# Performance work log

Measured on AMD Instinct MI355X. Metric: run time of the kernel, lower is better.

Reference implementation:

```python
import jax, jax.numpy as jnp
import numpy as np

B, S, H = 32, 512, 768
NHEAD, DH = 8, 96          # 8 heads * 96 = 768
E = 4096                   # edges per sample
NC = 2
NEG = -1e9
EPS = 1e-5


def _p(k, shape, scale=0.02):
    return scale * jax.random.normal(k, shape, dtype=jnp.float32)


def setup_inputs() -> dict:
    key = jax.random.key(0)
    ks = jax.random.split(key, 24)
    z = lambda *s: jnp.zeros(s, jnp.float32)
    return {
        "diff_encoded": jax.random.normal(ks[0], (B, S, H), jnp.float32),
        "msg_encoded": jax.random.normal(ks[1], (B, S, H), jnp.float32),
        "msg_mask": jnp.ones((B, S), jnp.int32),
        "edge_index_diff": jax.random.randint(ks[2], (B, 2, E), 0, S),
        "edge_index_msg": jax.random.randint(ks[3], (B, 2, E), 0, S),
        # GATv2Conv(heads=1): lin_l (source/message), lin_r (target), att vector, output bias
        "gat_wl": _p(ks[4], (H, H)), "gat_bl": z(H),
        "gat_wr": _p(ks[5], (H, H)), "gat_br": z(H),
        "gat_att": _p(ks[6], (H,)), "gat_bias": z(H),
        # cross MultiheadAttention
        "wq": _p(ks[7], (H, H)), "bq": z(H),
        "wk": _p(ks[8], (H, H)), "bk": z(H),
        "wv": _p(ks[9], (H, H)), "bv": z(H),
        "wo": _p(ks[10], (H, H)), "bo": z(H),
        # LayerNorm + MLP head
        "ln_g": jnp.ones((H,), jnp.float32), "ln_b": z(H),
        "fc0_w": _p(ks[11], (H, 512)), "fc0_b": z(512),
        "fc1_w": _p(ks[12], (512, 128)), "fc1_b": z(128),
        "fc2_w": _p(ks[13], (128, NC)), "fc2_b": z(NC),
    }


def _gat_single(x, edges, wl, bl, wr, br, att, bias):
    # GATv2Conv, heads=1, add_self_loops=True. x: [N,H], edges: [2,E] (src, dst).
    N = x.shape[0]
    src, dst = edges[0], edges[1]
    valid = (src < N) & (dst < N)            # clip_edge_index, as a mask
    src = jnp.where(valid, src, 0)
    dst = jnp.where(valid, dst, 0)
    loop = jnp.arange(N, dtype=src.dtype)    # PyG adds self loops
    src_a = jnp.concatenate([src, loop])
    dst_a = jnp.concatenate([dst, loop])
    valid_a = jnp.concatenate([valid, jnp.ones((N,), bool)])
    xl = x @ wl + bl                          # source / message transform
    xr = x @ wr + br                          # target transform
    e = jax.nn.leaky_relu(xl[src_a] + xr[dst_a], 0.2) @ att   # [E+N]
    e = jnp.where(valid_a, e, NEG)
    emax = jax.ops.segment_max(e, dst_a, num_segments=N)
    p = jnp.exp(e - emax[dst_a]) * valid_a.astype(x.dtype)
    denom = jax.ops.segment_sum(p, dst_a, num_segments=N)
    alpha = p / denom[dst_a]
    out = jax.ops.segment_sum(alpha[:, None] * xl[src_a], dst_a, num_segments=N)
    return out + bias


_gat = jax.vmap(_gat_single, in_axes=(0, 0) + (None,) * 6)


def _layernorm(x, g, b):
    mu = jnp.mean(x, -1, keepdims=True)
    var = jnp.mean(jnp.square(x - mu), -1, keepdims=True)
    return (x - mu) * jax.lax.rsqrt(var + EPS) * g + b


def reference(diff_encoded, msg_encoded, msg_mask, edge_index_diff, edge_index_msg,
              gat_wl, gat_bl, gat_wr, gat_br, gat_att, gat_bias,
              wq, bq, wk, bk, wv, bv, wo, bo, ln_g, ln_b,
              fc0_w, fc0_b, fc1_w, fc1_b, fc2_w, fc2_b):
    diff_g = _gat(diff_encoded, edge_index_diff, gat_wl, gat_bl, gat_wr, gat_br, gat_att, gat_bias) + diff_encoded
    msg_g = _gat(msg_encoded, edge_index_msg, gat_wl, gat_bl, gat_wr, gat_br, gat_att, gat_bias) + msg_encoded
    # cross attention: query=diff_g, key/value=msg_g, key_padding_mask = (msg_mask == 0)
    q = (diff_g @ wq + bq).reshape(B, S, NHEAD, DH)
    k = (msg_g @ wk + bk).reshape(B, S, NHEAD, DH)
    v = (msg_g @ wv + bv).reshape(B, S, NHEAD, DH)
    scores = jnp.einsum("bqhd,bkhd->bhqk", q, k) / jnp.sqrt(jnp.float32(DH))
    scores = jnp.where((msg_mask == 0)[:, None, None, :], NEG, scores)
    attn = jax.nn.softmax(scores, axis=-1)
    ctx = jnp.einsum("bhqk,bkhd->bqhd", attn, v).reshape(B, S, H) @ wo + bo
    fused = _layernorm(ctx + diff_g, ln_g, ln_b)
    x = fused[:, 0, :]                                  # CLS token
    x = jax.nn.relu(x @ fc0_w + fc0_b)                  # dropout = identity (eval)
    x = jax.nn.relu(x @ fc1_w + fc1_b)
    return x @ fc2_w + fc2_b
```

## Files before the change

### kernel.cpp

```cpp
#include <hip/hip_runtime.h>
#include <hip/hip_bf16.h>
#include <math.h>

#define BB 32
#define SS 512
#define HH 768
#define NHEADC 8
#define DHC 96
#define EE 4096
#define NCC 2
#define CAPC 128
#define CAP2 32
#define GSL 36
#define XRS 1536
#define NEGV -1000000000.0f
#define EPSV 1e-5f

#define PREP_CVT  12288
#define PREP_WT   2304
#define PREP_BIAS 3
#define PREP_CNT  512
#define PREP_TOT  (PREP_CVT + PREP_WT + PREP_BIAS + PREP_CNT)

typedef __hip_bfloat16 bf16;
typedef __bf16 bf16x8 __attribute__((ext_vector_type(8)));
typedef float f32x4 __attribute__((ext_vector_type(4)));

static __device__ inline unsigned short f2bf_u(float f) {
  __hip_bfloat16 h = __float2bfloat16(f);
  return *(unsigned short*)&h;
}
static __device__ inline float bfu(unsigned short u) {
  return __uint_as_float(((unsigned int)u) << 16);
}
static __device__ inline float bf2f(bf16 h) { return __bfloat162float(h); }

static __device__ inline void gload16(const void* g, void* l) {
  __builtin_amdgcn_global_load_lds(
      (const __attribute__((address_space(1))) void*)g,
      (__attribute__((address_space(3))) void*)l, 16, 0, 0);
}

__global__ __launch_bounds__(256) void k_prep(
    const float* __restrict__ msg_enc, bf16* __restrict__ Abf,
    const float* __restrict__ gat_wl, const float* __restrict__ gat_wr,
    const float* __restrict__ wk, const float* __restrict__ wv,
    bf16* __restrict__ wtA, bf16* __restrict__ wtB,
    const float* __restrict__ gat_bl, const float* __restrict__ gat_br,
    const float* __restrict__ bk, const float* __restrict__ bv,
    float* __restrict__ biasA, float* __restrict__ biasB,
    const int* __restrict__ e_msg, const int* __restrict__ e_diff,
    int* __restrict__ cnt, int* __restrict__ dcnt, int* __restrict__ dsrc)
{
  int blk = blockIdx.x, tid = threadIdx.x;
  if (blk < PREP_CVT) {
    int i = (blk * 256 + tid) * 4;
    float4 v = *(const float4*)(msg_enc + i);
    ushort4 o;
    o.x = f2bf_u(v.x); o.y = f2bf_u(v.y); o.z = f2bf_u(v.z); o.w = f2bf_u(v.w);
    *(ushort4*)((unsigned short*)Abf + i) = o;
    return;
  }
  blk -= PREP_CVT;
  if (blk < PREP_WT) {
    int z = blk / 576, rr = blk - z * 576;
    int bx = rr % 24, by = rr / 24;
    const float* w; bf16* o;
    switch (z) {
      case 0: w = gat_wl; o = wtA; break;
      case 1: w = gat_wr; o = wtA + (size_t)HH * HH; break;
      case 2: w = wk;     o = wtB; break;
      default: w = wv;    o = wtB + (size_t)HH * HH; break;
    }
    __shared__ float t[32][33];
    int n0 = bx * 32, k0 = by * 32;
    int x = tid & 31, y = tid >> 5;
    for (int yy = y; yy < 32; yy += 8)
      t[yy][x] = w[(size_t)(k0 + yy) * HH + n0 + x];
    __syncthreads();
    for (int yy = y; yy < 32; yy += 8)
      o[(size_t)(n0 + yy) * HH + k0 + x] = __float2bfloat16(t[x][yy]);
    return;
  }
  blk -= PREP_WT;
  if (blk < PREP_BIAS) {
    int t = blk * 256 + tid;
    if (t < HH) {
      biasA[t] = gat_bl[t]; biasA[HH + t] = gat_br[t];
      biasB[t] = bk[t];     biasB[HH + t] = bv[t];
    }
    return;
  }
  blk -= PREP_BIAS;
  {
    int i = blk * 256 + tid;
    if (i >= BB * EE) return;
    int b = i / EE, j = i - b * EE;
    int s = e_msg[b * 2 * EE + j], d = e_msg[b * 2 * EE + EE + j];
    if (s >= 0 && s < SS && d >= 0 && d < SS)
      atomicAdd(&cnt[b * SS + d], 1);
    int s2 = e_diff[b * 2 * EE + j], d2 = e_diff[b * 2 * EE + EE + j];
    if (s2 >= 0 && s2 < SS && d2 == 0) {
      int pos = atomicAdd(&dcnt[b], 1);
      if (pos < CAPC) dsrc[b * CAPC + pos] = s2;
    }
    if (j == 0) {
      int pos = atomicAdd(&dcnt[b], 1);
      if (pos < CAPC) dsrc[b * CAPC + pos] = 0;
    }
  }
}

template <typename OT>
__global__ __launch_bounds__(256) void k_gemm(
    const bf16* __restrict__ A, const bf16* __restrict__ Bt,
    const float* __restrict__ bias, OT* __restrict__ C,
    int M, int N, int K, int ldc)
{
  __shared__ __align__(16) bf16 As0[128 * 32];
  __shared__ __align__(16) bf16 As1[128 * 32];
  __shared__ __align__(16) bf16 Bs0[128 * 32];
  __shared__ __align__(16) bf16 Bs1[128 * 32];
  const int tid = threadIdx.x;
  const int wv = tid >> 6, lane = tid & 63;
  const int bm = blockIdx.x * 128, bn = blockIdx.y * 128;
  const int wm = (wv & 1) * 64, wn = (wv >> 1) * 64;
  const int m16 = lane & 15, half = lane >> 4;
  const int swz = (half ^ (m16 & 3)) * 8;
  f32x4 acc[4][4];
  #pragma unroll
  for (int i = 0; i < 4; ++i)
    #pragma unroll
    for (int j = 0; j < 4; ++j) acc[i][j] = (f32x4){0.f, 0.f, 0.f, 0.f};

  const int c0 = tid, c1 = tid + 256;
  const int r0 = c0 >> 2, o0 = (((c0 & 3) ^ ((c0 >> 2) & 3))) * 8;
  const int r1 = c1 >> 2, o1 = (((c1 & 3) ^ ((c1 >> 2) & 3))) * 8;
  const size_t aB0 = (size_t)(bm + r0) * K + o0;
  const size_t aB1 = (size_t)(bm + r1) * K + o1;
  const size_t bB0 = (size_t)(bn + r0) * K + o0;
  const size_t bB1 = (size_t)(bn + r1) * K + o1;

  for (int k0 = 0; k0 < K; k0 += 64) {
    __syncthreads();
    gload16(A + aB0 + k0, As0 + (size_t)c0 * 8);
    gload16(A + aB1 + k0, As0 + (size_t)c1 * 8);
    gload16(A + aB0 + k0 + 32, As1 + (size_t)c0 * 8);
    gload16(A + aB1 + k0 + 32, As1 + (size_t)c1 * 8);
    gload16(Bt + bB0 + k0, Bs0 + (size_t)c0 * 8);
    gload16(Bt + bB1 + k0, Bs0 + (size_t)c1 * 8);
    gload16(Bt + bB0 + k0 + 32, Bs1 + (size_t)c0 * 8);
    gload16(Bt + bB1 + k0 + 32, Bs1 + (size_t)c1 * 8);
    __syncthreads();
    #pragma unroll
    for (int ks = 0; ks < 2; ++ks) {
      const bf16* Ah = ks ? As1 : As0;
      const bf16* Bh = ks ? Bs1 : Bs0;
      bf16x8 af[4], bfv[4];
      #pragma unroll
      for (int t = 0; t < 4; ++t) {
        af[t]  = *(const bf16x8*)(Ah + (wm + t * 16 + m16) * 32 + swz);
        bfv[t] = *(const bf16x8*)(Bh + (wn + t * 16 + m16) * 32 + swz);
      }
      #pragma unroll
      for (int i = 0; i < 4; ++i)
        #pragma unroll
        for (int j = 0; j < 4; ++j)
          acc[i][j] = __builtin_amdgcn_mfma_f32_16x16x32_bf16(af[i], bfv[j], acc[i][j], 0, 0, 0);
    }
  }
  #pragma unroll
  for (int i = 0; i < 4; ++i) {
    #pragma unroll
    for (int j = 0; j < 4; ++j) {
      int col = bn + wn + j * 16 + m16;
      float bv = bias ? bias[col] : 0.f;
      #pragma unroll
      for (int r = 0; r < 4; ++r) {
        int row = bm + wm + i * 16 + half * 4 + r;
        float v = acc[i][j][r] + bv;
        if constexpr (sizeof(OT) == 2)
          C[(size_t)row * ldc + col] = (OT)__float2bfloat16(v);
        else
          C[(size_t)row * ldc + col] = v;
      }
    }
  }
}

__global__ __launch_bounds__(512) void k_scan(const int* __restrict__ cnt,
                                              int* __restrict__ offs,
                                              int* __restrict__ cursor) {
  __shared__ int tmp[SS];
  int b = blockIdx.x, t = threadIdx.x;
  int x = cnt[b * SS + t];
  tmp[t] = x;
  __syncthreads();
  for (int off = 1; off < SS; off <<= 1) {
    int u = (t >= off) ? tmp[t - off] : 0;
    __syncthreads();
    tmp[t] += u;
    __syncthreads();
  }
  int ex = tmp[t] - x;
  offs[b * SS + t] = ex;
  cursor[b * SS + t] = ex;
}

__global__ void k_scatter(const int* __restrict__ e_msg, int* __restrict__ cursor,
                          int* __restrict__ binned) {
  int i = blockIdx.x * blockDim.x + threadIdx.x;
  if (i >= BB * EE) return;
  int b = i / EE, j = i - b * EE;
  int s = e_msg[b * 2 * EE + j], d = e_msg[b * 2 * EE + EE + j];
  if (s >= 0 && s < SS && d >= 0 && d < SS) {
    int pos = atomicAdd(&cursor[b * SS + d], 1);
    binned[(size_t)b * EE + pos] = s;
  }
}

__global__ __launch_bounds__(256) void k_gat_fused(
    const int* __restrict__ binned, const int* __restrict__ offs,
    const int* __restrict__ cnt, const bf16* __restrict__ xlr,
    const float* __restrict__ att, const float* __restrict__ gbias,
    const bf16* __restrict__ resid, bf16* __restrict__ out)
{
  int bid = blockIdx.x;
  int xcd = bid & 7, idx = bid >> 3;
  int batch = xcd * 4 + (idx >> 7);
  int within = idx & 127;
  int lane = threadIdx.x & 63;
  int b = batch;
  int d = within * 4 + (threadIdx.x >> 6);
  int base = offs[b * SS + d], n = cnt[b * SS + d];
  const int* bin = binned + (size_t)b * EE + base;
  float av[12];
  {
    const float4* a4 = (const float4*)att;
    #pragma unroll
    for (int r = 0; r < 3; ++r) {
      float4 t = a4[lane + 64 * r];
      av[4*r] = t.x; av[4*r+1] = t.y; av[4*r+2] = t.z; av[4*r+3] = t.w;
    }
  }
  float xr[12];
  {
    const ushort4* p = (const ushort4*)(xlr + ((size_t)b * SS + d) * XRS + HH);
    #pragma unroll
    for (int r = 0; r < 3; ++r) {
      ushort4 v = p[lane + 64 * r];
      xr[4*r] = bfu(v.x); xr[4*r+1] = bfu(v.y); xr[4*r+2] = bfu(v.z); xr[4*r+3] = bfu(v.w);
    }
  }
  float m = -3.0e38f, l = 0.f;
  float acc[12] = {};
  for (int i = -1; i < n; ++i) {
    int s = (i < 0) ? d : bin[i];
    float xs[12];
    const ushort4* p = (const ushort4*)(xlr + ((size_t)b * SS + s) * XRS);
    #pragma unroll
    for (int r = 0; r < 3; ++r) {
      ushort4 v = p[lane + 64 * r];
      xs[4*r] = bfu(v.x); xs[4*r+1] = bfu(v.y); xs[4*r+2] = bfu(v.z); xs[4*r+3] = bfu(v.w);
    }
    float e = 0.f;
    #pragma unroll
    for (int k = 0; k < 12; ++k) {
      float t = xs[k] + xr[k];
      t = t > 0.f ? t : 0.2f * t;
      e += t * av[k];
    }
    #pragma unroll
    for (int off = 32; off > 0; off >>= 1) e += __shfl_xor(e, off);
    float mn = fmaxf(m, e);
    float so = __expf(m - mn);
    float w  = __expf(e - mn);
    l = l * so + w;
    #pragma unroll
    for (int k = 0; k < 12; ++k) acc[k] = acc[k] * so + w * xs[k];
    m = mn;
  }
  float inv = 1.f / l;
  size_t o = ((size_t)b * SS + d) * HH;
  const float4* gb4 = (const float4*)gbias;
  const ushort4* rs4 = (const ushort4*)(resid + o);
  ushort4* out4 = (ushort4*)(out + o);
  #pragma unroll
  for (int r = 0; r < 3; ++r) {
    int c = lane + 64 * r;
    float4 gg = gb4[c];
    ushort4 rr = rs4[c];
    ushort4 ov;
    ov.x = f2bf_u(acc[4*r+0] * inv + gg.x + bfu(rr.x));
    ov.y = f2bf_u(acc[4*r+1] * inv + gg.y + bfu(rr.y));
    ov.z = f2bf_u(acc[4*r+2] * inv + gg.z + bfu(rr.z));
    ov.w = f2bf_u(acc[4*r+3] * inv + gg.w + bfu(rr.w));
    out4[c] = ov;
  }
}

__global__ __launch_bounds__(192) void k_gather_diff(
    const int* __restrict__ dcnt, const int* __restrict__ dsrc,
    const float* __restrict__ diff_enc, bf16* __restrict__ G)
{
  int b = blockIdx.y, jj = blockIdx.x;
  int n = min(dcnt[b], CAP2);
  int t = threadIdx.x;
  size_t orow = ((size_t)b * GSL + jj) * HH;
  ushort4 o = {0, 0, 0, 0};
  if (jj < n || jj == CAP2) {
    int s = (jj == CAP2) ? 0 : dsrc[b * CAPC + jj];
    float4 v = ((const float4*)(diff_enc + ((size_t)b * SS + s) * HH))[t];
    o.x = f2bf_u(v.x); o.y = f2bf_u(v.y); o.z = f2bf_u(v.z); o.w = f2bf_u(v.w);
  }
  *(ushort4*)((unsigned short*)G + orow + t * 4) = o;
}

__global__ __launch_bounds__(256) void k_diff_gat0(
    const int* __restrict__ dcnt, const float* __restrict__ GD,
    const float* __restrict__ att, const float* __restrict__ gbias,
    const float* __restrict__ diff_enc, float* __restrict__ dg0)
{
  int b = blockIdx.x;
  int n = min(dcnt[b], CAP2);
  __shared__ float ee[CAP2];
  __shared__ float al[CAP2];
  __shared__ float xr0s[HH];
  int wave = threadIdx.x >> 6, lane = threadIdx.x & 63;
  for (int h = threadIdx.x; h < HH; h += 256)
    xr0s[h] = GD[((size_t)b * GSL + CAP2) * XRS + HH + h];
  __syncthreads();
  for (int jj = wave; jj < n; jj += 4) {
    const float* px = GD + ((size_t)b * GSL + jj) * XRS;
    float part = 0.f;
    #pragma unroll
    for (int r = 0; r < HH / 64; ++r) {
      int h = lane + 64 * r;
      float t = px[h] + xr0s[h];
      t = t > 0.f ? t : 0.2f * t;
      part += t * att[h];
    }
    #pragma unroll
    for (int off = 32; off > 0; off >>= 1) part += __shfl_xor(part, off);
    if (lane == 0) ee[jj] = part;
  }
  __syncthreads();
  if (threadIdx.x == 0) {
    float m = -3.0e38f;
    for (int i = 0; i < n; ++i) m = fmaxf(m, ee[i]);
    float ssum = 0.f;
    for (int i = 0; i < n; ++i) ssum += expf(ee[i] - m);
    float inv = 1.f / ssum;
    for (int i = 0; i < n; ++i) al[i] = expf(ee[i] - m) * inv;
  }
  __syncthreads();
  for (int h = threadIdx.x; h < HH; h += 256) {
    float acc = 0.f;
    for (int i = 0; i < n; ++i) acc += al[i] * GD[((size_t)b * GSL + i) * XRS + h];
    dg0[b * HH + h] = acc + gbias[h] + diff_enc[(size_t)b * SS * HH + h];
  }
}

__global__ __launch_bounds__(256) void k_colmat(
    const float* __restrict__ in, const float* __restrict__ w,
    const float* __restrict__ bias, const float* __restrict__ extra,
    float* __restrict__ outp, int Kd, int Nd, long in_stride, int relu)
{
  int b = blockIdx.y, n0 = blockIdx.x * 64;
  int tid = threadIdx.x, wv = tid >> 6, lane = tid & 63;
  __shared__ float xs[HH];
  __shared__ float red[4][64];
  const float* src = in + (size_t)b * in_stride;
  for (int k = tid; k < Kd; k += 256) xs[k] = src[k];
  __syncthreads();
  int h = n0 + lane;
  int kpw = Kd >> 2;
  int kb = wv * kpw;
  float acc = 0.f;
  for (int k = 0; k < kpw; k += 8) {
    #pragma unroll
    for (int u = 0; u < 8; ++u) {
      int kk = kb + k + u;
      acc += xs[kk] * w[(size_t)kk * Nd + h];
    }
  }
  red[wv][lane] = acc;
  __syncthreads();
  if (tid < 64) {
    float s = red[0][tid] + red[1][tid] + red[2][tid] + red[3][tid] + bias[n0 + tid];
    if (extra) s += extra[(size_t)b * Nd + n0 + tid];
    if (relu) s = fmaxf(s, 0.f);
    outp[(size_t)b * Nd + n0 + tid] = s;
  }
}

__global__ __launch_bounds__(256) void k_ln(
    const float* __restrict__ xin, const float* __restrict__ g,
    const float* __restrict__ bta, float* __restrict__ yout)
{
  int b = blockIdx.x, tid = threadIdx.x;
  __shared__ float red[4], redq[4];
  float v0 = xin[b * HH + tid];
  float v1 = xin[b * HH + tid + 256];
  float v2 = xin[b * HH + tid + 512];
  float sum = v0 + v1 + v2;
  float sq = v0 * v0 + v1 * v1 + v2 * v2;
  #pragma unroll
  for (int off = 32; off > 0; off >>= 1) { sum += __shfl_xor(sum, off); sq += __shfl_xor(sq, off); }
  int wv = tid >> 6, lane = tid & 63;
  if (lane == 0) { red[wv] = sum; redq[wv] = sq; }
  __syncthreads();
  sum = red[0] + red[1] + red[2] + red[3];
  sq = redq[0] + redq[1] + redq[2] + redq[3];
  float mu = sum / HH;
  float var = sq / HH - mu * mu;
  float scl = rsqrtf(var + EPSV);
  yout[b * HH + tid]       = (v0 - mu) * scl * g[tid]       + bta[tid];
  yout[b * HH + tid + 256] = (v1 - mu) * scl * g[tid + 256] + bta[tid + 256];
  yout[b * HH + tid + 512] = (v2 - mu) * scl * g[tid + 512] + bta[tid + 512];
}

__global__ __launch_bounds__(256) void k_fc12(
    const float* __restrict__ a0g, const float* __restrict__ fc1w,
    const float* __restrict__ fc1b, const float* __restrict__ fc2w,
    const float* __restrict__ fc2b, float* __restrict__ out)
{
  int b = blockIdx.x, tid = threadIdx.x;
  __shared__ float a0s[512];
  __shared__ float a1s[128];
  __shared__ float r1[2][128];
  for (int k = tid; k < 512; k += 256) a0s[k] = a0g[b * 512 + k];
  __syncthreads();
  int o = tid & 127, hf = tid >> 7;
  int kb = hf * 256;
  float acc = 0.f;
  for (int k = 0; k < 256; k += 8) {
    #pragma unroll
    for (int u = 0; u < 8; ++u) {
      int kk = kb + k + u;
      acc += a0s[kk] * fc1w[(size_t)kk * 128 + o];
    }
  }
  r1[hf][o] = acc;
  __syncthreads();
  if (tid < 128) a1s[tid] = fmaxf(r1[0][tid] + r1[1][tid] + fc1b[tid], 0.f);
  __syncthreads();
  if (tid < 128) {
    int oo = tid >> 6, l = tid & 63;
    float p = a1s[l] * fc2w[l * 2 + oo] + a1s[l + 64] * fc2w[(l + 64) * 2 + oo];
    #pragma unroll
    for (int off = 32; off > 0; off >>= 1) p += __shfl_xor(p, off);
    if (l == 0) out[b * NCC + oo] = p + fc2b[oo];
  }
}

__global__ __launch_bounds__(512) void k_attn(
    const float* __restrict__ q0, const bf16* __restrict__ kvb,
    const int* __restrict__ mask, float* __restrict__ ctx)
{
  int b = blockIdx.x / NHEADC, hd = blockIdx.x % NHEADC;
  __shared__ float qs[DHC];
  __shared__ float sc[SS];
  __shared__ float redm[8];
  __shared__ float reds[8];
  __shared__ float pr4[4][DHC];
  int tid = threadIdx.x;
  if (tid < DHC) qs[tid] = q0[b * HH + hd * DHC + tid];
  __syncthreads();
  const float scale = 0.10206207261596575f;
  {
    int s = tid;
    const int4* pk4 = (const int4*)(kvb + ((size_t)b * SS + s) * XRS + hd * DHC);
    float acc = 0.f;
    #pragma unroll
    for (int c = 0; c < 12; ++c) {
      int4 raw = pk4[c];
      const unsigned short* u = (const unsigned short*)&raw;
      #pragma unroll
      for (int j = 0; j < 8; ++j) acc += qs[c * 8 + j] * bfu(u[j]);
    }
    sc[s] = (mask[b * SS + s] != 0) ? acc * scale : NEGV;
  }
  __syncthreads();
  int wave = tid >> 6, lane = tid & 63;
  float m = sc[tid];
  #pragma unroll
  for (int off = 32; off > 0; off >>= 1) m = fmaxf(m, __shfl_xor(m, off));
  if (lane == 0) redm[wave] = m;
  __syncthreads();
  m = redm[0];
  #pragma unroll
  for (int i = 1; i < 8; ++i) m = fmaxf(m, redm[i]);
  float p0 = expf(sc[tid] - m);
  float ssum = p0;
  #pragma unroll
  for (int off = 32; off > 0; off >>= 1) ssum += __shfl_xor(ssum, off);
  if (lane == 0) reds[wave] = ssum;
  __syncthreads();
  ssum = reds[0] + reds[1] + reds[2] + reds[3] + reds[4] + reds[5] + reds[6] + reds[7];
  float inv = 1.f / ssum;
  sc[tid] = p0 * inv;
  __syncthreads();
  {
    int hs = tid >> 7, d = tid & 127;
    if (d < DHC) {
      const bf16* pv = kvb + ((size_t)b * SS + hs * 128) * XRS + HH + hd * DHC + d;
      float acc = 0.f;
      for (int s = 0; s < 128; s += 8) {
        #pragma unroll
        for (int u = 0; u < 8; ++u)
          acc += sc[hs * 128 + s + u] * bf2f(pv[(size_t)(s + u) * XRS]);
      }
      pr4[hs][d] = acc;
    }
  }
  __syncthreads();
  if (tid < DHC)
    ctx[b * HH + hd * DHC + tid] = pr4[0][tid] + pr4[1][tid] + pr4[2][tid] + pr4[3][tid];
}

extern "C" void kernel_launch(void* const* d_in, const int* in_sizes, int n_in,
                              void* d_out, int out_size, void* d_ws, size_t ws_size,
                              hipStream_t stream) {
  const float* diff_enc = (const float*)d_in[0];
  const float* msg_enc  = (const float*)d_in[1];
  const int*   msg_mask = (const int*)d_in[2];
  const int*   e_diff   = (const int*)d_in[3];
  const int*   e_msg    = (const int*)d_in[4];
  const float* gat_wl   = (const float*)d_in[5];
  const float* gat_bl   = (const float*)d_in[6];
  const float* gat_wr   = (const float*)d_in[7];
  const float* gat_br   = (const float*)d_in[8];
  const float* gat_att  = (const float*)d_in[9];
  const float* gat_bias = (const float*)d_in[10];
  const float* wq = (const float*)d_in[11];
  const float* bq = (const float*)d_in[12];
  const float* wk = (const float*)d_in[13];
  const float* bk = (const float*)d_in[14];
  const float* wv = (const float*)d_in[15];
  const float* bv = (const float*)d_in[16];
  const float* wo = (const float*)d_in[17];
  const float* bo = (const float*)d_in[18];
  const float* ln_g = (const float*)d_in[19];
  const float* ln_b = (const float*)d_in[20];
  const float* fc0w = (const float*)d_in[21];
  const float* fc0b = (const float*)d_in[22];
  const float* fc1w = (const float*)d_in[23];
  const float* fc1b = (const float*)d_in[24];
  const float* fc2w = (const float*)d_in[25];
  const float* fc2b = (const float*)d_in[26];
  float* out = (float*)d_out;

  char* ws = (char*)d_ws;
  size_t off = 0;
  auto alloc = [&](size_t bytes) -> void* {
    void* p = (void*)(ws + off);
    off += (bytes + 255) & ~(size_t)255;
    return p;
  };
  bf16* Abf    = (bf16*)alloc((size_t)BB * SS * HH * 2);
  bf16* xlr    = (bf16*)alloc((size_t)BB * SS * XRS * 2);
  bf16* kv     = (bf16*)alloc((size_t)BB * SS * XRS * 2);
  bf16* mg     = (bf16*)alloc((size_t)BB * SS * HH * 2);
  bf16* wtA    = (bf16*)alloc((size_t)2 * HH * HH * 2);
  bf16* wtB    = (bf16*)alloc((size_t)2 * HH * HH * 2);
  float* biasA = (float*)alloc((size_t)XRS * 4);
  float* biasB = (float*)alloc((size_t)XRS * 4);
  int*   cnt   = (int*)alloc((size_t)BB * SS * 4);
  int*   offs  = (int*)alloc((size_t)BB * SS * 4);
  int*   cursor= (int*)alloc((size_t)BB * SS * 4);
  int*   binned= (int*)alloc((size_t)BB * EE * 4);
  bf16*  G     = (bf16*)alloc((size_t)BB * GSL * HH * 2);
  float* GD    = (float*)alloc((size_t)BB * GSL * XRS * 4);
  int*   dcnt  = (int*)alloc((size_t)BB * 4);
  int*   dsrc  = (int*)alloc((size_t)BB * CAPC * 4);
  float* dg0   = (float*)alloc((size_t)BB * HH * 4);
  float* q0    = (float*)alloc((size_t)BB * HH * 4);
  float* ctx   = (float*)alloc((size_t)BB * HH * 4);
  float* fpre  = (float*)alloc((size_t)BB * HH * 4);
  float* fnrm  = (float*)alloc((size_t)BB * HH * 4);
  float* a0g   = (float*)alloc((size_t)BB * 512 * 4);

  hipMemsetAsync(cnt, 0, (size_t)BB * SS * 4, stream);
  hipMemsetAsync(dcnt, 0, (size_t)BB * 4, stream);

  k_prep<<<PREP_TOT, 256, 0, stream>>>(msg_enc, Abf, gat_wl, gat_wr, wk, wv,
                                       wtA, wtB, gat_bl, gat_br, bk, bv,
                                       biasA, biasB, e_msg, e_diff,
                                       cnt, dcnt, dsrc);
  k_scan<<<BB, SS, 0, stream>>>(cnt, offs, cursor);
  k_scatter<<<(BB * EE + 255) / 256, 256, 0, stream>>>(e_msg, cursor, binned);

  dim3 gBlk(256), gGridA((BB * SS) / 128, XRS / 128);
  k_gemm<bf16><<<gGridA, gBlk, 0, stream>>>(Abf, wtA, biasA, xlr,
                                            BB * SS, XRS, HH, XRS);
  k_gat_fused<<<(BB * SS) / 4, 256, 0, stream>>>(binned, offs, cnt, xlr,
                                                 gat_att, gat_bias, Abf, mg);
  k_gemm<bf16><<<gGridA, gBlk, 0, stream>>>(mg, wtB, biasB, kv,
                                            BB * SS, XRS, HH, XRS);
  {
    dim3 gg(GSL, BB);
    k_gather_diff<<<gg, 192, 0, stream>>>(dcnt, dsrc, diff_enc, G);
    dim3 gGridD((BB * GSL) / 128, XRS / 128);
    k_gemm<float><<<gGridD, gBlk, 0, stream>>>(G, wtA, biasA, GD,
                                               BB * GSL, XRS, HH, XRS);
  }
  k_diff_gat0<<<BB, 256, 0, stream>>>(dcnt, GD, gat_att, gat_bias, diff_enc, dg0);
  {
    dim3 g(HH / 64, BB);
    k_colmat<<<g, 256, 0, stream>>>(dg0, wq, bq, nullptr, q0, HH, HH, HH, 0);
  }
  k_attn<<<BB * NHEADC, 512, 0, stream>>>(q0, kv, msg_mask, ctx);
  {
    dim3 g(HH / 64, BB);
    k_colmat<<<g, 256, 0, stream>>>(ctx, wo, bo, dg0, fpre, HH, HH, HH, 0);
  }
  k_ln<<<BB, 256, 0, stream>>>(fpre, ln_g, ln_b, fnrm);
  {
    dim3 g(512 / 64, BB);
    k_colmat<<<g, 256, 0, stream>>>(fnrm, fc0w, fc0b, nullptr, a0g, HH, 512, HH, 1);
  }
  k_fc12<<<BB, 256, 0, stream>>>(a0g, fc1w, fc1b, fc2w, fc2b, out);
}
```

Baseline: 441.1 us.

## Split fused xl/xr and k/v buffers, prefetch GAT source rows, drop LDS swizzle

The GEMM epilogue now writes the two halves of each 1536-wide output into separate 768-stride buffers (xl/xr, k/v, GDl/GDr), so consumer kernels read compact rows. The GAT aggregation loop software-prefetches the next source row's features one iteration ahead to hide gather latency. The XOR swizzle in the GEMM's shared-memory tile addressing is removed, which simplifies index math but may bring back LDS bank conflicts on the fragment loads.

```diff
diff --git a/kernel.cpp b/kernel.cpp
--- a/kernel.cpp
+++ b/kernel.cpp
@@ -12,7 +12,6 @@
 #define CAPC 128
 #define CAP2 32
 #define GSL 36
-#define XRS 1536
 #define NEGV -1000000000.0f
 #define EPSV 1e-5f
 
@@ -114,8 +113,8 @@
 template <typename OT>
 __global__ __launch_bounds__(256) void k_gemm(
     const bf16* __restrict__ A, const bf16* __restrict__ Bt,
-    const float* __restrict__ bias, OT* __restrict__ C,
-    int M, int N, int K, int ldc)
+    const float* __restrict__ bias, OT* __restrict__ C0, OT* __restrict__ C1,
+    int M, int K)
 {
   __shared__ __align__(16) bf16 As0[128 * 32];
   __shared__ __align__(16) bf16 As1[128 * 32];
@@ -126,7 +125,6 @@
   const int bm = blockIdx.x * 128, bn = blockIdx.y * 128;
   const int wm = (wv & 1) * 64, wn = (wv >> 1) * 64;
   const int m16 = lane & 15, half = lane >> 4;
-  const int swz = (half ^ (m16 & 3)) * 8;
   f32x4 acc[4][4];
   #pragma unroll
   for (int i = 0; i < 4; ++i)
@@ -134,8 +132,8 @@
     for (int j = 0; j < 4; ++j) acc[i][j] = (f32x4){0.f, 0.f, 0.f, 0.f};
 
   const int c0 = tid, c1 = tid + 256;
-  const int r0 = c0 >> 2, o0 = (((c0 & 3) ^ ((c0 >> 2) & 3))) * 8;
-  const int r1 = c1 >> 2, o1 = (((c1 & 3) ^ ((c1 >> 2) & 3))) * 8;
+  const int r0 = c0 >> 2, o0 = (c0 & 3) * 8;
+  const int r1 = c1 >> 2, o1 = (c1 & 3) * 8;
   const size_t aB0 = (size_t)(bm + r0) * K + o0;
   const size_t aB1 = (size_t)(bm + r1) * K + o1;
   const size_t bB0 = (size_t)(bn + r0) * K + o0;
@@ -159,8 +157,8 @@
       bf16x8 af[4], bfv[4];
       #pragma unroll
       for (int t = 0; t < 4; ++t) {
-        af[t]  = *(const bf16x8*)(Ah + (wm + t * 16 + m16) * 32 + swz);
-        bfv[t] = *(const bf16x8*)(Bh + (wn + t * 16 + m16) * 32 + swz);
+        af[t]  = *(const bf16x8*)(Ah + (wm + t * 16 + m16) * 32 + half * 8);
+        bfv[t] = *(const bf16x8*)(Bh + (wn + t * 16 + m16) * 32 + half * 8);
       }
       #pragma unroll
       for (int i = 0; i < 4; ++i)
@@ -175,14 +173,16 @@
     for (int j = 0; j < 4; ++j) {
       int col = bn + wn + j * 16 + m16;
       float bv = bias ? bias[col] : 0.f;
+      OT* Cb = (col < HH) ? C0 : C1;
+      int cc = (col < HH) ? col : col - HH;
       #pragma unroll
       for (int r = 0; r < 4; ++r) {
         int row = bm + wm + i * 16 + half * 4 + r;
         float v = acc[i][j][r] + bv;
         if constexpr (sizeof(OT) == 2)
-          C[(size_t)row * ldc + col] = (OT)__float2bfloat16(v);
+          Cb[(size_t)row * HH + cc] = (OT)__float2bfloat16(v);
         else
-          C[(size_t)row * ldc + col] = v;
+          Cb[(size_t)row * HH + cc] = v;
       }
     }
   }
@@ -221,17 +221,16 @@
 
 __global__ __launch_bounds__(256) void k_gat_fused(
     const int* __restrict__ binned, const int* __restrict__ offs,
-    const int* __restrict__ cnt, const bf16* __restrict__ xlr,
-    const float* __restrict__ att, const float* __restrict__ gbias,
-    const bf16* __restrict__ resid, bf16* __restrict__ out)
+    const int* __restrict__ cnt, const bf16* __restrict__ xl,
+    const bf16* __restrict__ xrb, const float* __restrict__ att,
+    const float* __restrict__ gbias, const bf16* __restrict__ resid,
+    bf16* __restrict__ out)
 {
   int bid = blockIdx.x;
   int xcd = bid & 7, idx = bid >> 3;
-  int batch = xcd * 4 + (idx >> 7);
-  int within = idx & 127;
+  int b = xcd * 4 + (idx >> 7);
+  int d = (idx & 127) * 4 + (threadIdx.x >> 6);
   int lane = threadIdx.x & 63;
-  int b = batch;
-  int d = within * 4 + (threadIdx.x >> 6);
   int base = offs[b * SS + d], n = cnt[b * SS + d];
   const int* bin = binned + (size_t)b * EE + base;
   float av[12];
@@ -245,7 +244,7 @@
   }
   float xr[12];
   {
-    const ushort4* p = (const ushort4*)(xlr + ((size_t)b * SS + d) * XRS + HH);
+    const ushort4* p = (const ushort4*)(xrb + ((size_t)b * SS + d) * HH);
     #pragma unroll
     for (int r = 0; r < 3; ++r) {
       ushort4 v = p[lane + 64 * r];
@@ -254,15 +253,23 @@
   }
   float m = -3.0e38f, l = 0.f;
   float acc[12] = {};
-  for (int i = -1; i < n; ++i) {
-    int s = (i < 0) ? d : bin[i];
+  int nn = n + 1;
+  ushort4 pre[3];
+  {
+    const ushort4* p = (const ushort4*)(xl + ((size_t)b * SS + d) * HH);
+    pre[0] = p[lane]; pre[1] = p[lane + 64]; pre[2] = p[lane + 128];
+  }
+  for (int j = 0; j < nn; ++j) {
+    ushort4 cur0 = pre[0], cur1 = pre[1], cur2 = pre[2];
+    if (j + 1 < nn) {
+      int sn = bin[j];
+      const ushort4* p = (const ushort4*)(xl + ((size_t)b * SS + sn) * HH);
+      pre[0] = p[lane]; pre[1] = p[lane + 64]; pre[2] = p[lane + 128];
+    }
     float xs[12];
-    const ushort4* p = (const ushort4*)(xlr + ((size_t)b * SS + s) * XRS);
-    #pragma unroll
-    for (int r = 0; r < 3; ++r) {
-      ushort4 v = p[lane + 64 * r];
-      xs[4*r] = bfu(v.x); xs[4*r+1] = bfu(v.y); xs[4*r+2] = bfu(v.z); xs[4*r+3] = bfu(v.w);
-    }
+    xs[0] = bfu(cur0.x); xs[1] = bfu(cur0.y); xs[2]  = bfu(cur0.z); xs[3]  = bfu(cur0.w);
+    xs[4] = bfu(cur1.x); xs[5] = bfu(cur1.y); xs[6]  = bfu(cur1.z); xs[7]  = bfu(cur1.w);
+    xs[8] = bfu(cur2.x); xs[9] = bfu(cur2.y); xs[10] = bfu(cur2.z); xs[11] = bfu(cur2.w);
     float e = 0.f;
     #pragma unroll
     for (int k = 0; k < 12; ++k) {
@@ -317,9 +324,10 @@
 }
 
 __global__ __launch_bounds__(256) void k_diff_gat0(
-    const int* __restrict__ dcnt, const float* __restrict__ GD,
-    const float* __restrict__ att, const float* __restrict__ gbias,
-    const float* __restrict__ diff_enc, float* __restrict__ dg0)
+    const int* __restrict__ dcnt, const float* __restrict__ GDl,
+    const float* __restrict__ GDr, const float* __restrict__ att,
+    const float* __restrict__ gbias, const float* __restrict__ diff_enc,
+    float* __restrict__ dg0)
 {
   int b = blockIdx.x;
   int n = min(dcnt[b], CAP2);
@@ -328,10 +336,10 @@
   __shared__ float xr0s[HH];
   int wave = threadIdx.x >> 6, lane = threadIdx.x & 63;
   for (int h = threadIdx.x; h < HH; h += 256)
-    xr0s[h] = GD[((size_t)b * GSL + CAP2) * XRS + HH + h];
+    xr0s[h] = GDr[((size_t)b * GSL + CAP2) * HH + h];
   __syncthreads();
   for (int jj = wave; jj < n; jj += 4) {
-    const float* px = GD + ((size_t)b * GSL + jj) * XRS;
+    const float* px = GDl + ((size_t)b * GSL + jj) * HH;
     float part = 0.f;
     #pragma unroll
     for (int r = 0; r < HH / 64; ++r) {
@@ -356,7 +364,7 @@
   __syncthreads();
   for (int h = threadIdx.x; h < HH; h += 256) {
     float acc = 0.f;
-    for (int i = 0; i < n; ++i) acc += al[i] * GD[((size_t)b * GSL + i) * XRS + h];
+    for (int i = 0; i < n; ++i) acc += al[i] * GDl[((size_t)b * GSL + i) * HH + h];
     dg0[b * HH + h] = acc + gbias[h] + diff_enc[(size_t)b * SS * HH + h];
   }
 }
@@ -455,8 +463,9 @@
 }
 
 __global__ __launch_bounds__(512) void k_attn(
-    const float* __restrict__ q0, const bf16* __restrict__ kvb,
-    const int* __restrict__ mask, float* __restrict__ ctx)
+    const float* __restrict__ q0, const bf16* __restrict__ kb,
+    const bf16* __restrict__ vb, const int* __restrict__ mask,
+    float* __restrict__ ctx)
 {
   int b = blockIdx.x / NHEADC, hd = blockIdx.x % NHEADC;
   __shared__ float qs[DHC];
@@ -470,7 +479,7 @@
   const float scale = 0.10206207261596575f;
   {
     int s = tid;
-    const int4* pk4 = (const int4*)(kvb + ((size_t)b * SS + s) * XRS + hd * DHC);
+    const int4* pk4 = (const int4*)(kb + ((size_t)b * SS + s) * HH + hd * DHC);
     float acc = 0.f;
     #pragma unroll
     for (int c = 0; c < 12; ++c) {
@@ -504,12 +513,12 @@
   {
     int hs = tid >> 7, d = tid & 127;
     if (d < DHC) {
-      const bf16* pv = kvb + ((size_t)b * SS + hs * 128) * XRS + HH + hd * DHC + d;
+      const bf16* pv = vb + ((size_t)b * SS + hs * 128) * HH + hd * DHC + d;
       float acc = 0.f;
       for (int s = 0; s < 128; s += 8) {
         #pragma unroll
         for (int u = 0; u < 8; ++u)
-          acc += sc[hs * 128 + s + u] * bf2f(pv[(size_t)(s + u) * XRS]);
+          acc += sc[hs * 128 + s + u] * bf2f(pv[(size_t)(s + u) * HH]);
       }
       pr4[hs][d] = acc;
     }
@@ -559,19 +568,22 @@
     return p;
   };
   bf16* Abf    = (bf16*)alloc((size_t)BB * SS * HH * 2);
-  bf16* xlr    = (bf16*)alloc((size_t)BB * SS * XRS * 2);
-  bf16* kv     = (bf16*)alloc((size_t)BB * SS * XRS * 2);
+  bf16* xl     = (bf16*)alloc((size_t)BB * SS * HH * 2);
+  bf16* xrb    = (bf16*)alloc((size_t)BB * SS * HH * 2);
+  bf16* kbuf   = (bf16*)alloc((size_t)BB * SS * HH * 2);
+  bf16* vbuf   = (bf16*)alloc((size_t)BB * SS * HH * 2);
   bf16* mg     = (bf16*)alloc((size_t)BB * SS * HH * 2);
   bf16* wtA    = (bf16*)alloc((size_t)2 * HH * HH * 2);
   bf16* wtB    = (bf16*)alloc((size_t)2 * HH * HH * 2);
-  float* biasA = (float*)alloc((size_t)XRS * 4);
-  float* biasB = (float*)alloc((size_t)XRS * 4);
+  float* biasA = (float*)alloc((size_t)2 * HH * 4);
+  float* biasB = (float*)alloc((size_t)2 * HH * 4);
   int*   cnt   = (int*)alloc((size_t)BB * SS * 4);
   int*   offs  = (int*)alloc((size_t)BB * SS * 4);
   int*   cursor= (int*)alloc((size_t)BB * SS * 4);
   int*   binned= (int*)alloc((size_t)BB * EE * 4);
   bf16*  G     = (bf16*)alloc((size_t)BB * GSL * HH * 2);
-  float* GD    = (float*)alloc((size_t)BB * GSL * XRS * 4);
+  float* GDl   = (float*)alloc((size_t)BB * GSL * HH * 4);
+  float* GDr   = (float*)alloc((size_t)BB * GSL * HH * 4);
   int*   dcnt  = (int*)alloc((size_t)BB * 4);
   int*   dsrc  = (int*)alloc((size_t)BB * CAPC * 4);
   float* dg0   = (float*)alloc((size_t)BB * HH * 4);
@@ -591,26 +603,23 @@
   k_scan<<<BB, SS, 0, stream>>>(cnt, offs, cursor);
   k_scatter<<<(BB * EE + 255) / 256, 256, 0, stream>>>(e_msg, cursor, binned);
 
-  dim3 gBlk(256), gGridA((BB * SS) / 128, XRS / 128);
-  k_gemm<bf16><<<gGridA, gBlk, 0, stream>>>(Abf, wtA, biasA, xlr,
-                                            BB * SS, XRS, HH, XRS);
-  k_gat_fused<<<(BB * SS) / 4, 256, 0, stream>>>(binned, offs, cnt, xlr,
+  dim3 gBlk(256), gGridA((BB * SS) / 128, (2 * HH) / 128);
+  k_gemm<bf16><<<gGridA, gBlk, 0, stream>>>(Abf, wtA, biasA, xl, xrb, BB * SS, HH);
+  k_gat_fused<<<(BB * SS) / 4, 256, 0, stream>>>(binned, offs, cnt, xl, xrb,
                                                  gat_att, gat_bias, Abf, mg);
-  k_gemm<bf16><<<gGridA, gBlk, 0, stream>>>(mg, wtB, biasB, kv,
-                                            BB * SS, XRS, HH, XRS);
+  k_gemm<bf16><<<gGridA, gBlk, 0, stream>>>(mg, wtB, biasB, kbuf, vbuf, BB * SS, HH);
   {
     dim3 gg(GSL, BB);
     k_gather_diff<<<gg, 192, 0, stream>>>(dcnt, dsrc, diff_enc, G);
-    dim3 gGridD((BB * GSL) / 128, XRS / 128);
-    k_gemm<float><<<gGridD, gBlk, 0, stream>>>(G, wtA, biasA, GD,
-                                               BB * GSL, XRS, HH, XRS);
-  }
-  k_diff_gat0<<<BB, 256, 0, stream>>>(dcnt, GD, gat_att, gat_bias, diff_enc, dg0);
+    dim3 gGridD((BB * GSL) / 128, (2 * HH) / 128);
+    k_gemm<float><<<gGridD, gBlk, 0, stream>>>(G, wtA, biasA, GDl, GDr, BB * GSL, HH);
+  }
+  k_diff_gat0<<<BB, 256, 0, stream>>>(dcnt, GDl, GDr, gat_att, gat_bias, diff_enc, dg0);
   {
     dim3 g(HH / 64, BB);
     k_colmat<<<g, 256, 0, stream>>>(dg0, wq, bq, nullptr, q0, HH, HH, HH, 0);
   }
-  k_attn<<<BB * NHEADC, 512, 0, stream>>>(q0, kv, msg_mask, ctx);
+  k_attn<<<BB * NHEADC, 512, 0, stream>>>(q0, kbuf, vbuf, msg_mask, ctx);
   {
     dim3 g(HH / 64, BB);
     k_colmat<<<g, 256, 0, stream>>>(ctx, wo, bo, dg0, fpre, HH, HH, HH, 0);
```

After: 435.3 us. Within noise of the previous version (-1.3%).
